# Optimization experiments

Hardware: AMD Instinct MI355X
Metric: run time of the kernel (lower is better)

Reference implementation:

```python
import jax, jax.numpy as jnp
import numpy as np

TOPK = 13
NUM_CLASSES = 80
ALPHA = 1.0
BETA = 6.0
EPS = 1e-9
IMG = 640.0


def _make_boxes(key, lead_shape, img=IMG):
    k1, k2 = jax.random.split(key)
    cxy = jax.random.uniform(k1, lead_shape + (2,), minval=0.0, maxval=img)
    wh = jax.random.uniform(k2, lead_shape + (2,), minval=8.0, maxval=128.0)
    return jnp.concatenate([cxy - wh / 2, cxy + wh / 2], axis=-1)  # valid xyxy


def setup_inputs() -> dict:
    key = jax.random.key(0)
    ks = jax.random.split(key, 6)
    bs, na, n, nc = 16, 8400, 64, NUM_CLASSES
    pd_scores = jax.random.uniform(ks[0], (bs, na, nc), dtype=jnp.float32)
    pd_bboxes = _make_boxes(ks[1], (bs, na))
    anc_points = jax.random.uniform(ks[2], (na, 2), minval=0.0, maxval=IMG)
    gt_labels = jax.random.randint(ks[3], (bs, n, 1), 0, nc, dtype=jnp.int64 if jax.config.jax_enable_x64 else jnp.int32)
    gt_bboxes = _make_boxes(ks[4], (bs, n))
    mask_gt = (jax.random.uniform(ks[5], (bs, n, 1)) < 0.8).astype(jnp.float32)
    return dict(pd_scores=pd_scores, pd_bboxes=pd_bboxes, anc_points=anc_points,
                gt_labels=gt_labels, gt_bboxes=gt_bboxes, mask_gt=mask_gt)


def _bbox_ciou(box1, box2, eps=1e-7):
    # box1, box2: (..., 4) xyxy, broadcastable. Matches ultralytics bbox_iou(CIoU=True).
    b1x1, b1y1, b1x2, b1y2 = (box1[..., i] for i in range(4))
    b2x1, b2y1, b2x2, b2y2 = (box2[..., i] for i in range(4))
    w1, h1 = b1x2 - b1x1, b1y2 - b1y1 + eps
    w2, h2 = b2x2 - b2x1, b2y2 - b2y1 + eps
    inter = (jnp.clip(jnp.minimum(b1x2, b2x2) - jnp.maximum(b1x1, b2x1), 0.0)
             * jnp.clip(jnp.minimum(b1y2, b2y2) - jnp.maximum(b1y1, b2y1), 0.0))
    union = w1 * h1 + w2 * h2 - inter + eps
    iou = inter / union
    cw = jnp.maximum(b1x2, b2x2) - jnp.minimum(b1x1, b2x1)  # enclosing box
    ch = jnp.maximum(b1y2, b2y2) - jnp.minimum(b1y1, b2y1)
    c2 = cw * cw + ch * ch + eps
    rho2 = ((b2x1 + b2x2 - b1x1 - b1x2) ** 2 + (b2y1 + b2y2 - b1y1 - b1y2) ** 2) / 4.0
    v = (4.0 / (jnp.pi ** 2)) * (jnp.arctan(w2 / h2) - jnp.arctan(w1 / h1)) ** 2
    alpha = jax.lax.stop_gradient(v / (v - iou + (1.0 + eps)))  # torch.no_grad() in original
    return iou - (rho2 / c2 + v * alpha)


def _assign(pd_scores, pd_bboxes, anc_points, gt_labels, gt_bboxes, mask_gt):
    bs, na, nc = pd_scores.shape
    n = gt_bboxes.shape[1]
    # --- select_candidates_in_gts: anchor center strictly inside gt box ---
    lt = gt_bboxes[:, :, None, :2]                    # (bs,n,1,2)
    rb = gt_bboxes[:, :, None, 2:]
    ap = anc_points[None, None]                       # (1,1,na,2)
    deltas = jnp.concatenate([ap - lt, rb - ap], -1)  # (bs,n,na,4)
    mask_in_gts = (deltas.min(-1) > EPS).astype(pd_bboxes.dtype)  # (bs,n,na)
    mask = (mask_in_gts * mask_gt) > 0                # (bs,n,na) bool
    # --- get_box_metrics ---
    lbl = gt_labels.squeeze(-1).astype(jnp.int32)     # (bs,n)
    scores_t = jnp.transpose(pd_scores, (0, 2, 1))    # (bs,nc,na)
    bbox_scores = scores_t[jnp.arange(bs)[:, None], lbl]          # (bs,n,na)
    bbox_scores = jnp.where(mask, bbox_scores, 0.0)
    ciou = _bbox_ciou(gt_bboxes[:, :, None, :], pd_bboxes[:, None, :, :])  # (bs,n,na)
    overlaps = jnp.where(mask, jnp.clip(ciou, 0.0), 0.0)
    align_metric = (bbox_scores ** ALPHA) * (overlaps ** BETA)
    # --- select_topk_candidates ---
    _, topk_idxs = jax.lax.top_k(align_metric, TOPK)  # (bs,n,TOPK)
    topk_mask = jnp.broadcast_to(mask_gt > 0, (bs, n, TOPK))
    topk_idxs = jnp.where(topk_mask, topk_idxs, 0)
    bi = jnp.arange(bs)[:, None, None]
    ni = jnp.arange(n)[None, :, None]
    counts = jnp.zeros((bs, n, na), jnp.int32).at[bi, ni, topk_idxs].add(1)
    mask_topk = jnp.where(counts > 1, 0, counts).astype(align_metric.dtype)
    mask_pos = mask_topk * mask_in_gts * mask_gt      # (bs,n,na)
    # --- select_highest_overlaps: one gt per anchor ---
    fg_mask = mask_pos.sum(-2)                        # (bs,na)
    max_ov_idx = overlaps.argmax(1)                   # (bs,na)
    is_max = jnp.transpose(jax.nn.one_hot(max_ov_idx, n, dtype=mask_pos.dtype), (0, 2, 1))
    mask_pos = jnp.where(fg_mask[:, None, :] > 1, is_max, mask_pos)
    fg_mask = mask_pos.sum(-2)
    target_gt_idx = mask_pos.argmax(-2)               # (bs,na)
    # --- get_targets ---
    flat_idx = target_gt_idx + jnp.arange(bs)[:, None] * n
    target_labels = jnp.clip(gt_labels.reshape(-1)[flat_idx], 0)  # (bs,na)
    target_bboxes = gt_bboxes.reshape(-1, 4)[flat_idx]            # (bs,na,4)
    target_scores = jax.nn.one_hot(target_labels, nc, dtype=pd_scores.dtype)
    target_scores = jnp.where(fg_mask[..., None] > 0, target_scores, 0.0)
    # --- normalize by aligned metric ---
    align_metric = align_metric * mask_pos
    pos_align = align_metric.max(-1, keepdims=True)               # (bs,n,1)
    pos_ov = (overlaps * mask_pos).max(-1, keepdims=True)         # (bs,n,1)
    norm = (align_metric * pos_ov / (pos_align + EPS)).max(-2)[..., None]  # (bs,na,1)
    target_scores = target_scores * norm
    return target_labels, target_bboxes, target_scores, fg_mask > 0, target_gt_idx


def reference(pd_scores, pd_bboxes, anc_points, gt_labels, gt_bboxes, mask_gt):
    return _assign(pd_scores, pd_bboxes, anc_points, gt_labels, gt_bboxes, mask_gt)
```

## Files before the change

kernel.cpp:

```cpp
#include <hip/hip_runtime.h>
#include <math.h>

#define BS   16
#define NA   8400
#define NGT  64
#define NC   80
#define TK   13
#define CAP  1024
#define NCHUNK ((NA + 255) / 256)
#define EPSA 1e-9f
#define EPSC 1e-7f

typedef unsigned long long u64;

__device__ __forceinline__ u64 umax64(u64 a, u64 b) { return a > b ? a : b; }
__device__ __forceinline__ u64 umin64(u64 a, u64 b) { return a < b ? a : b; }

__device__ __forceinline__ u64 shfl_xor_u64(u64 v, int m) {
    int lo = __shfl_xor((int)(unsigned)v, m, 64);
    int hi = __shfl_xor((int)(unsigned)(v >> 32), m, 64);
    return ((u64)(unsigned)hi << 32) | (unsigned)lo;
}

__device__ __forceinline__ void merge16(u64* t, const u64* o) {
    u64 c[16];
#pragma unroll
    for (int i = 0; i < 16; ++i) c[i] = umax64(t[i], o[15 - i]);
#pragma unroll
    for (int d = 8; d >= 1; d >>= 1) {
#pragma unroll
        for (int i = 0; i < 16; ++i) {
            if ((i & d) == 0) {
                u64 hi = umax64(c[i], c[i + d]);
                u64 lo = umin64(c[i], c[i + d]);
                c[i] = hi; c[i + d] = lo;
            }
        }
    }
#pragma unroll
    for (int i = 0; i < 16; ++i) t[i] = c[i];
}

__device__ __forceinline__ void insert13(u64* t, u64 key) {
    u64 cur = key;
#pragma unroll
    for (int s = 0; s < 13; ++s) {
        u64 hi = umax64(t[s], cur);
        cur    = umin64(t[s], cur);
        t[s]   = hi;
    }
}

__device__ __forceinline__ float ciou_clip(float4 g, float4 p, float at1, float a1) {
    float w2 = p.z - p.x;
    float h2 = p.w - p.y + EPSC;
    float iw = fminf(g.z, p.z) - fmaxf(g.x, p.x);
    float ih = fminf(g.w, p.w) - fmaxf(g.y, p.y);
    float inter = fmaxf(iw, 0.f) * fmaxf(ih, 0.f);
    float uni   = a1 + w2 * h2 - inter + EPSC;
    float iou   = inter / uni;
    float cw = fmaxf(g.z, p.z) - fminf(g.x, p.x);
    float ch = fmaxf(g.w, p.w) - fminf(g.y, p.y);
    float c2 = cw * cw + ch * ch + EPSC;
    float dx = p.x + p.z - g.x - g.z;
    float dy = p.y + p.w - g.y - g.w;
    float rho2 = (dx * dx + dy * dy) * 0.25f;
    float dat  = atanf(w2 / h2) - at1;
    float v    = (4.0f / (float)(M_PI * M_PI)) * dat * dat;
    float alpha = v / (v - iou + (1.0f + EPSC));
    float ciou  = iou - (rho2 / c2 + v * alpha);
    return fmaxf(ciou, 0.f);
}

__global__ __launch_bounds__(256) void k1_pairs(
        const float* __restrict__ pd_scores,
        const float* __restrict__ pd_bboxes,
        const float* __restrict__ anc,
        const int*   __restrict__ gt_labels,
        const float* __restrict__ gt_bboxes,
        const float* __restrict__ mask_gt,
        u64* __restrict__ cand,
        int* __restrict__ cnt,
        unsigned char* __restrict__ amax_idx) {
    int bx = blockIdx.x;
    int b  = bx / NCHUNK;
    int a  = (bx % NCHUNK) * 256 + threadIdx.x;

    __shared__ float4 sg[NGT];
    __shared__ float  sat1[NGT], sa1[NGT], smgt[NGT];
    __shared__ int    slbl[NGT];
    if (threadIdx.x < NGT) {
        int j = threadIdx.x, bj = b * NGT + j;
        float4 g = ((const float4*)gt_bboxes)[bj];
        sg[j] = g;
        float w1 = g.z - g.x, h1 = g.w - g.y + EPSC;
        sat1[j] = atanf(w1 / h1);
        sa1[j]  = w1 * h1;
        smgt[j] = mask_gt[bj];
        slbl[j] = gt_labels[bj];
    }
    __syncthreads();
    if (a >= NA) return;

    float2 ap = ((const float2*)anc)[a];
    float4 p  = ((const float4*)pd_bboxes)[(size_t)b * NA + a];
    const float* sbase = pd_scores + (size_t)b * NA * NC + (size_t)a * NC;

    float bv = 0.f; int bi = 0;
    for (int j = 0; j < NGT; ++j) {
        float4 g = sg[j];
        float dmin = fminf(fminf(ap.x - g.x, ap.y - g.y),
                           fminf(g.z - ap.x, g.w - ap.y));
        bool act    = smgt[j] > 0.f;
        bool inside = dmin > EPSA;
        float o = 0.f;
        if (act && inside) {
            o = ciou_clip(g, p, sat1[j], sa1[j]);
            float sc = sbase[slbl[j]];
            float o2 = o * o;
            float al = sc * (o2 * o2 * o2);
            u64 key = ((u64)__float_as_uint(al) << 32) |
                      (u64)(((unsigned)(16384 - a) << 1) | 1u);
            int bj = b * NGT + j;
            int pos = atomicAdd(&cnt[bj], 1);
            if (pos < CAP) cand[(size_t)bj * CAP + pos] = key;
        } else if (act && a < 16) {
            u64 key = (u64)((unsigned)(16384 - a) << 1);
            int bj = b * NGT + j;
            int pos = atomicAdd(&cnt[bj], 1);
            if (pos < CAP) cand[(size_t)bj * CAP + pos] = key;
        }
        if (o > bv) { bv = o; bi = j; }
    }
    amax_idx[(size_t)b * NA + a] = (unsigned char)bi;
}

__global__ __launch_bounds__(256) void k2_topk(
        const u64* __restrict__ cand,
        const int* __restrict__ cnt,
        u64* __restrict__ bits) {
    int bj   = blockIdx.x * 4 + (threadIdx.x >> 6);
    int lane = threadIdx.x & 63;
    int b = bj >> 6, j = bj & 63;
    int n = cnt[bj]; if (n > CAP) n = CAP;
    const u64* lst = cand + (size_t)bj * CAP;

    u64 t[16];
#pragma unroll
    for (int i = 0; i < 16; ++i) t[i] = 0;
    for (int i = lane; i < n; i += 64) insert13(t, lst[i]);

#pragma unroll
    for (int d = 1; d < 64; d <<= 1) {
        u64 o16[16];
#pragma unroll
        for (int i = 0; i < 16; ++i) o16[i] = shfl_xor_u64(t[i], d);
        merge16(t, o16);
    }
    if (lane == 0) {
        u64 mybit = 1ULL << j;
#pragma unroll
        for (int it = 0; it < TK; ++it) {
            unsigned low = (unsigned)t[it];
            int a = 16384 - (int)(low >> 1);
            if (low & 1u)
                atomicOr(&bits[(size_t)b * NA + a], mybit);
        }
    }
}

__global__ __launch_bounds__(256) void k3_resolve(
        const float* __restrict__ pd_scores,
        const float* __restrict__ pd_bboxes,
        const float* __restrict__ anc,
        const int*   __restrict__ gt_labels,
        const float* __restrict__ gt_bboxes,
        const float* __restrict__ mask_gt,
        const u64* __restrict__ bits,
        const unsigned char* __restrict__ amax_idx,
        float* __restrict__ out_labels,
        float* __restrict__ out_bboxes,
        float* __restrict__ out_fg,
        float* __restrict__ out_tgt,
        float* __restrict__ al_res,
        unsigned* __restrict__ pos_align_u,
        unsigned* __restrict__ pos_ov_u) {
    int bx = blockIdx.x;
    int b  = bx / NCHUNK;
    int a  = (bx % NCHUNK) * 256 + threadIdx.x;

    __shared__ float4 sg[NGT];
    __shared__ float  sat1[NGT], sa1[NGT], smgt[NGT];
    __shared__ int    slbl[NGT];
    if (threadIdx.x < NGT) {
        int j = threadIdx.x, bj = b * NGT + j;
        float4 g = ((const float4*)gt_bboxes)[bj];
        sg[j] = g;
        float w1 = g.z - g.x, h1 = g.w - g.y + EPSC;
        sat1[j] = atanf(w1 / h1);
        sa1[j]  = w1 * h1;
        smgt[j] = mask_gt[bj];
        slbl[j] = gt_labels[bj];
    }
    __syncthreads();
    if (a >= NA) return;

    size_t i = (size_t)b * NA + a;
    u64 mb = bits[i];
    int fg = __popcll(mb);
    int tgt;
    if (fg > 1)      tgt = amax_idx[i];
    else if (fg == 1) tgt = __ffsll((unsigned long long)mb) - 1;
    else             tgt = 0;

    float al = 0.f;
    if (fg > 0) {
        float4 g = sg[tgt];
        float2 ap = ((const float2*)anc)[a];
        float dmin = fminf(fminf(ap.x - g.x, ap.y - g.y),
                           fminf(g.z - ap.x, g.w - ap.y));
        if (smgt[tgt] > 0.f && dmin > EPSA) {
            float4 p = ((const float4*)pd_bboxes)[(size_t)b * NA + a];
            float o  = ciou_clip(g, p, sat1[tgt], sa1[tgt]);
            float sc = pd_scores[(size_t)b * NA * NC + (size_t)a * NC + slbl[tgt]];
            float o2 = o * o;
            al = sc * (o2 * o2 * o2);
            atomicMax(&pos_ov_u[b * NGT + tgt], __float_as_uint(o));
        }
        atomicMax(&pos_align_u[b * NGT + tgt], __float_as_uint(al));
    }
    al_res[i] = al;

    int lbl = slbl[tgt]; if (lbl < 0) lbl = 0;
    out_labels[i] = (float)lbl;
    ((float4*)out_bboxes)[i] = sg[tgt];
    out_fg[i]  = (fg > 0) ? 1.f : 0.f;
    out_tgt[i] = (float)tgt;
}

__global__ __launch_bounds__(256) void k5_scores(
        const float* __restrict__ al_res,
        const float* __restrict__ out_labels,
        const float* __restrict__ out_fg,
        const float* __restrict__ out_tgt,
        const float* __restrict__ pos_align,
        const float* __restrict__ pos_ov,
        float* __restrict__ out_scores) {
    int i4 = blockIdx.x * blockDim.x + threadIdx.x;
    if (i4 >= BS * NA * (NC / 4)) return;
    int ba = i4 / (NC / 4);
    int c0 = (i4 - ba * (NC / 4)) * 4;
    float nm = 0.f; int lbl = -1;
    if (out_fg[ba] > 0.f) {
        int b   = ba / NA;
        int tgt = (int)out_tgt[ba];
        int bj  = b * NGT + tgt;
        nm  = al_res[ba] * pos_ov[bj] / (pos_align[bj] + EPSA);
        lbl = (int)out_labels[ba];
    }
    float4 v;
    v.x = (lbl == c0    ) ? nm : 0.f;
    v.y = (lbl == c0 + 1) ? nm : 0.f;
    v.z = (lbl == c0 + 2) ? nm : 0.f;
    v.w = (lbl == c0 + 3) ? nm : 0.f;
    ((float4*)out_scores)[i4] = v;
}

extern "C" void kernel_launch(void* const* d_in, const int* in_sizes, int n_in,
                              void* d_out, int out_size, void* d_ws, size_t ws_size,
                              hipStream_t stream) {
    const float* pd_scores = (const float*)d_in[0];
    const float* pd_bboxes = (const float*)d_in[1];
    const float* anc       = (const float*)d_in[2];
    const int*   gt_labels = (const int*)d_in[3];
    const float* gt_bboxes = (const float*)d_in[4];
    const float* mask_gt   = (const float*)d_in[5];

    char* p = (char*)d_ws;
    u64*      bits        = (u64*)p;      p += (size_t)BS * NA * sizeof(u64);
    int*      cnt         = (int*)p;      p += (size_t)BS * NGT * sizeof(int);
    unsigned* pos_align_u = (unsigned*)p; p += (size_t)BS * NGT * sizeof(unsigned);
    unsigned* pos_ov_u    = (unsigned*)p; p += (size_t)BS * NGT * sizeof(unsigned);
    size_t zbytes = (size_t)(p - (char*)d_ws);
    u64*   cand   = (u64*)p;   p += (size_t)BS * NGT * CAP * sizeof(u64);
    float* al_res = (float*)p; p += (size_t)BS * NA * sizeof(float);
    unsigned char* amax_idx = (unsigned char*)p; p += (size_t)BS * NA;

    float* out_labels = (float*)d_out;
    float* out_bboxes = out_labels + (size_t)BS * NA;
    float* out_scores = out_bboxes + (size_t)BS * NA * 4;
    float* out_fg     = out_scores + (size_t)BS * NA * NC;
    float* out_tgt    = out_fg     + (size_t)BS * NA;

    hipMemsetAsync(d_ws, 0, zbytes, stream);

    k1_pairs<<<BS * NCHUNK, 256, 0, stream>>>(pd_scores, pd_bboxes, anc, gt_labels,
                                              gt_bboxes, mask_gt, cand, cnt, amax_idx);
    k2_topk<<<BS * NGT / 4, 256, 0, stream>>>(cand, cnt, bits);
    k3_resolve<<<BS * NCHUNK, 256, 0, stream>>>(pd_scores, pd_bboxes, anc, gt_labels,
                                                gt_bboxes, mask_gt, bits, amax_idx,
                                                out_labels, out_bboxes, out_fg, out_tgt,
                                                al_res, pos_align_u, pos_ov_u);
    k5_scores<<<(BS * NA * (NC / 4) + 255) / 256, 256, 0, stream>>>(
        al_res, out_labels, out_fg, out_tgt,
        (const float*)pos_align_u, (const float*)pos_ov_u, out_scores);
}
```

Before: 89.40 us.

## Remap pair kernel so each wave lane handles one GT over an anchor slice

The pair kernel now assigns one GT box per lane and has each 64-lane wave loop over a contiguous slice of anchors. Previously each thread owned an anchor and looped over all 64 GTs. Per-GT constants live in registers instead of shared memory. The per-anchor argmax over GTs becomes a wave ballot plus a shuffle reduction, skipped when at most one lane overlaps. This removes per-thread divergence across GTs and the scattered atomics from different anchors. The cost is a serial anchor loop per wave, uncoalesced per-anchor score loads with the label varying by lane, and a reduction on every anchor that has multiple hits.

```diff
diff --git a/kernel.cpp b/kernel.cpp
--- a/kernel.cpp
+++ b/kernel.cpp
@@ -7,6 +7,8 @@
 #define NC   80
 #define TK   13
 #define CAP  1024
+#define WPB  512
+#define AW   ((NA + WPB - 1) / WPB)
 #define NCHUNK ((NA + 255) / 256)
 #define EPSA 1e-9f
 #define EPSC 1e-7f
@@ -82,57 +84,60 @@
         u64* __restrict__ cand,
         int* __restrict__ cnt,
         unsigned char* __restrict__ amax_idx) {
-    int bx = blockIdx.x;
-    int b  = bx / NCHUNK;
-    int a  = (bx % NCHUNK) * 256 + threadIdx.x;
-
-    __shared__ float4 sg[NGT];
-    __shared__ float  sat1[NGT], sa1[NGT], smgt[NGT];
-    __shared__ int    slbl[NGT];
-    if (threadIdx.x < NGT) {
-        int j = threadIdx.x, bj = b * NGT + j;
-        float4 g = ((const float4*)gt_bboxes)[bj];
-        sg[j] = g;
-        float w1 = g.z - g.x, h1 = g.w - g.y + EPSC;
-        sat1[j] = atanf(w1 / h1);
-        sa1[j]  = w1 * h1;
-        smgt[j] = mask_gt[bj];
-        slbl[j] = gt_labels[bj];
-    }
-    __syncthreads();
-    if (a >= NA) return;
-
-    float2 ap = ((const float2*)anc)[a];
-    float4 p  = ((const float4*)pd_bboxes)[(size_t)b * NA + a];
-    const float* sbase = pd_scores + (size_t)b * NA * NC + (size_t)a * NC;
-
-    float bv = 0.f; int bi = 0;
-    for (int j = 0; j < NGT; ++j) {
-        float4 g = sg[j];
+    int wg   = blockIdx.x * 4 + (threadIdx.x >> 6);
+    int b    = wg / WPB;
+    int w    = wg - b * WPB;
+    int lane = threadIdx.x & 63;
+    int bj   = b * NGT + lane;
+
+    float4 g   = ((const float4*)gt_bboxes)[bj];
+    float  mgt = mask_gt[bj];
+    int    lbl = gt_labels[bj];
+    float w1 = g.z - g.x, h1 = g.w - g.y + EPSC;
+    float at1 = atanf(w1 / h1);
+    float a1  = w1 * h1;
+    bool act  = mgt > 0.f;
+
+    const float4* pbb = ((const float4*)pd_bboxes) + (size_t)b * NA;
+    const float*  psc = pd_scores + (size_t)b * NA * NC;
+
+    int a0   = w * AW;
+    int aend = a0 + AW; if (aend > NA) aend = NA;
+
+    for (int a = a0; a < aend; ++a) {
+        float2 ap = ((const float2*)anc)[a];
+        float4 p  = pbb[a];
         float dmin = fminf(fminf(ap.x - g.x, ap.y - g.y),
                            fminf(g.z - ap.x, g.w - ap.y));
-        bool act    = smgt[j] > 0.f;
         bool inside = dmin > EPSA;
         float o = 0.f;
         if (act && inside) {
-            o = ciou_clip(g, p, sat1[j], sa1[j]);
-            float sc = sbase[slbl[j]];
+            o = ciou_clip(g, p, at1, a1);
+            float sc = psc[(size_t)a * NC + lbl];
             float o2 = o * o;
             float al = sc * (o2 * o2 * o2);
             u64 key = ((u64)__float_as_uint(al) << 32) |
                       (u64)(((unsigned)(16384 - a) << 1) | 1u);
-            int bj = b * NGT + j;
             int pos = atomicAdd(&cnt[bj], 1);
             if (pos < CAP) cand[(size_t)bj * CAP + pos] = key;
         } else if (act && a < 16) {
             u64 key = (u64)((unsigned)(16384 - a) << 1);
-            int bj = b * NGT + j;
             int pos = atomicAdd(&cnt[bj], 1);
             if (pos < CAP) cand[(size_t)bj * CAP + pos] = key;
         }
-        if (o > bv) { bv = o; bi = j; }
-    }
-    amax_idx[(size_t)b * NA + a] = (unsigned char)bi;
+
+        u64 pb = __ballot(o > 0.f);
+        int idx;
+        if (__popcll(pb) <= 1) {
+            idx = pb ? (__ffsll(pb) - 1) : 0;
+        } else {
+            u64 k = ((u64)__float_as_uint(o) << 6) | (unsigned)(63 - lane);
+#pragma unroll
+            for (int d = 1; d < 64; d <<= 1) k = umax64(k, shfl_xor_u64(k, d));
+            idx = 63 - (int)(k & 63ULL);
+        }
+        if (lane == 0) amax_idx[(size_t)b * NA + a] = (unsigned char)idx;
+    }
 }
 
 __global__ __launch_bounds__(256) void k2_topk(
@@ -209,9 +214,9 @@
     u64 mb = bits[i];
     int fg = __popcll(mb);
     int tgt;
-    if (fg > 1)      tgt = amax_idx[i];
-    else if (fg == 1) tgt = __ffsll((unsigned long long)mb) - 1;
-    else             tgt = 0;
+    if (fg > 1)       tgt = amax_idx[i];
+    else if (fg == 1) tgt = __ffsll(mb) - 1;
+    else              tgt = 0;
 
     float al = 0.f;
     if (fg > 0) {
@@ -294,8 +299,8 @@
 
     hipMemsetAsync(d_ws, 0, zbytes, stream);
 
-    k1_pairs<<<BS * NCHUNK, 256, 0, stream>>>(pd_scores, pd_bboxes, anc, gt_labels,
-                                              gt_bboxes, mask_gt, cand, cnt, amax_idx);
+    k1_pairs<<<BS * WPB / 4, 256, 0, stream>>>(pd_scores, pd_bboxes, anc, gt_labels,
+                                               gt_bboxes, mask_gt, cand, cnt, amax_idx);
     k2_topk<<<BS * NGT / 4, 256, 0, stream>>>(cand, cnt, bits);
     k3_resolve<<<BS * NCHUNK, 256, 0, stream>>>(pd_scores, pd_bboxes, anc, gt_labels,
                                                 gt_bboxes, mask_gt, bits, amax_idx,
```

Result: faster. 72.35 us (-19.1%).
